# Kernel optimization log

Hardware: AMD Instinct MI355X
Metric: run time of the kernel (lower is better)

## Reference

```python
import jax, jax.numpy as jnp
import numpy as np


def setup_inputs() -> dict:
    key = jax.random.key(0)
    B, C, T = 64, 256, 2048
    X = jax.random.normal(key, (B, C, T), dtype=jnp.float32)
    return {"X": X}


def reference(X) -> jnp.ndarray:
    # torch.cov(correction=0) per sample: rows = variables, cols = observations
    T = X.shape[-1]
    Xc = X - jnp.mean(X, axis=-1, keepdims=True)      # [B, C, T]
    cov = jnp.einsum('bct,bdt->bcd', Xc, Xc) / T       # [B, C, C]
    return cov
```

## Files before the change

kernel.cpp:

```cpp
#include <hip/hip_runtime.h>


#define NB 64
#define NC 256
#define NT 2048
#define NITER 32

typedef __bf16 bf16x8 __attribute__((ext_vector_type(8)));
typedef float  f32x8  __attribute__((ext_vector_type(8)));
typedef float  f32x4  __attribute__((ext_vector_type(4)));

__global__ __launch_bounds__(512, 2) void cov_kernel(const float* __restrict__ X,
                                                     float* __restrict__ out) {
    __shared__ __align__(16) unsigned char smem[68608];
    __bf16* sAB  = (__bf16*)smem;
    float*  redF = (float*)smem;

    const int bid  = blockIdx.x;
    const int xcd  = bid & 7;
    const int g    = bid >> 3;
    const int b    = xcd + 8 * (g >> 2);
    const int q    = g & 3;
    const int row0 = (q >> 1) * 128, col0 = (q & 1) * 128;

    const float* __restrict__ Xb = X + (size_t)b * (NC * NT);

    const int t    = threadIdx.x;
    const int lane = t & 63;
    const int wave = t >> 6;
    const int h    = wave >> 2;
    const int wq   = wave & 3;
    const int wm   = wq >> 1, wn = wq & 1;
    const int quad = lane >> 4;
    const int l16  = lane & 15;

    const int u  = t & 255;
    const int sr = u >> 2;
    const int sc = (u & 3) * 8;
    const float* gA0 = Xb + (size_t)(row0 + sr) * NT + h * (NT / 2) + sc;
    const float* gA1 = gA0 + (size_t)64 * NT;
    const float* gB0 = Xb + (size_t)(col0 + sr) * NT + h * (NT / 2) + sc;
    const float* gB1 = gB0 + (size_t)64 * NT;

    __bf16* sA[2] = { sAB + (0 * 2 + h) * 4096, sAB + (1 * 2 + h) * 4096 };
    __bf16* sB[2] = { sAB + 16384 + (0 * 2 + h) * 4096, sAB + 16384 + (1 * 2 + h) * 4096 };
    const int woff = sr * 32 + sc;

    f32x4 acc[4][4], accRS[4], accCS[4];
#pragma unroll
    for (int i = 0; i < 4; ++i) {
        accRS[i] = (f32x4){0.f, 0.f, 0.f, 0.f};
        accCS[i] = (f32x4){0.f, 0.f, 0.f, 0.f};
#pragma unroll
        for (int j = 0; j < 4; ++j) acc[i][j] = (f32x4){0.f, 0.f, 0.f, 0.f};
    }
    const bf16x8 ones = {(__bf16)1.0f, (__bf16)1.0f, (__bf16)1.0f, (__bf16)1.0f,
                         (__bf16)1.0f, (__bf16)1.0f, (__bf16)1.0f, (__bf16)1.0f};

    f32x8 pA0 = *(const f32x8*)gA0;
    f32x8 pA1 = *(const f32x8*)gA1;
    f32x8 pB0 = *(const f32x8*)gB0;
    f32x8 pB1 = *(const f32x8*)gB1;
    *(bf16x8*)(sA[0] + woff)        = __builtin_convertvector(pA0, bf16x8);
    *(bf16x8*)(sA[0] + woff + 2048) = __builtin_convertvector(pA1, bf16x8);
    *(bf16x8*)(sB[0] + woff)        = __builtin_convertvector(pB0, bf16x8);
    *(bf16x8*)(sB[0] + woff + 2048) = __builtin_convertvector(pB1, bf16x8);
    pA0 = *(const f32x8*)(gA0 + 32);
    pA1 = *(const f32x8*)(gA1 + 32);
    pB0 = *(const f32x8*)(gB0 + 32);
    pB1 = *(const f32x8*)(gB1 + 32);
    __syncthreads();

    const int aBase = (wm * 64 + l16) * 32 + quad * 8;
    const int bBase = (wn * 64 + l16) * 32 + quad * 8;

#pragma unroll 2
    for (int k = 0; k < NITER; ++k) {
        const int cur = k & 1, nxt = cur ^ 1;

        if (k + 1 < NITER) {
            *(bf16x8*)(sA[nxt] + woff)        = __builtin_convertvector(pA0, bf16x8);
            *(bf16x8*)(sA[nxt] + woff + 2048) = __builtin_convertvector(pA1, bf16x8);
            *(bf16x8*)(sB[nxt] + woff)        = __builtin_convertvector(pB0, bf16x8);
            *(bf16x8*)(sB[nxt] + woff + 2048) = __builtin_convertvector(pB1, bf16x8);
        }
        if (k + 2 < NITER) {
            pA0 = *(const f32x8*)(gA0 + (k + 2) * 32);
            pA1 = *(const f32x8*)(gA1 + (k + 2) * 32);
            pB0 = *(const f32x8*)(gB0 + (k + 2) * 32);
            pB1 = *(const f32x8*)(gB1 + (k + 2) * 32);
        }

        bf16x8 aF[4], bF[4];
#pragma unroll
        for (int mt = 0; mt < 4; ++mt)
            aF[mt] = *(const bf16x8*)(sA[cur] + aBase + mt * 16 * 32);
#pragma unroll
        for (int nt = 0; nt < 4; ++nt)
            bF[nt] = *(const bf16x8*)(sB[cur] + bBase + nt * 16 * 32);

#pragma unroll
        for (int mt = 0; mt < 4; ++mt) {
            accRS[mt] = __builtin_amdgcn_mfma_f32_16x16x32_bf16(aF[mt], ones, accRS[mt], 0, 0, 0);
#pragma unroll
            for (int nt = 0; nt < 4; ++nt)
                acc[mt][nt] = __builtin_amdgcn_mfma_f32_16x16x32_bf16(aF[mt], bF[nt], acc[mt][nt], 0, 0, 0);
        }
#pragma unroll
        for (int nt = 0; nt < 4; ++nt)
            accCS[nt] = __builtin_amdgcn_mfma_f32_16x16x32_bf16(ones, bF[nt], accCS[nt], 0, 0, 0);

        __syncthreads();
    }

    float* red = redF + wq * (64 * 65);
    float* rs  = redF + 4 * (64 * 65);
    float* cs  = rs + 256;

    if (h == 1) {
#pragma unroll
        for (int mt = 0; mt < 4; ++mt)
#pragma unroll
            for (int nt = 0; nt < 4; ++nt)
#pragma unroll
                for (int r = 0; r < 4; ++r)
                    red[(mt * 16 + quad * 4 + r) * 65 + nt * 16 + l16] = acc[mt][nt][r];
        if (l16 == 0) {
#pragma unroll
            for (int mt = 0; mt < 4; ++mt)
#pragma unroll
                for (int r = 0; r < 4; ++r)
                    rs[wq * 64 + mt * 16 + quad * 4 + r] = accRS[mt][r];
        }
        if (quad == 0) {
#pragma unroll
            for (int nt = 0; nt < 4; ++nt)
                cs[wq * 64 + nt * 16 + l16] = accCS[nt][0];
        }
    }
    __syncthreads();

    if (h == 0) {
        const float invT = 1.0f / NT;
        float* __restrict__ outB = out + (size_t)b * (NC * NC);
#pragma unroll
        for (int mt = 0; mt < 4; ++mt) {
#pragma unroll
            for (int nt = 0; nt < 4; ++nt) {
#pragma unroll
                for (int r = 0; r < 4; ++r) {
                    const int R = mt * 16 + quad * 4 + r;
                    const int C = nt * 16 + l16;
                    const float tot = red[R * 65 + C] + acc[mt][nt][r];
                    const float Sx  = rs[wq * 64 + R] + accRS[mt][r];
                    const float Sy  = cs[wq * 64 + C] + accCS[nt][0];
                    outB[(size_t)(row0 + wm * 64 + R) * NC + (col0 + wn * 64 + C)] =
                        (tot - Sx * Sy * invT) * invT;
                }
            }
        }
    }
}

extern "C" void kernel_launch(void* const* d_in, const int* in_sizes, int n_in,
                              void* d_out, int out_size, void* d_ws, size_t ws_size,
                              hipStream_t stream) {
    const float* X = (const float*)d_in[0];
    float* out = (float*)d_out;
    (void)in_sizes; (void)n_in; (void)out_size; (void)d_ws; (void)ws_size;
    cov_kernel<<<256, 512, 0, stream>>>(X, out);
}
```

Before: 205.4 us.

## Split-K Gram over full 256x256 tiles with a separate reduction kernel

Each block now computes the full 256x256 Gram matrix for one batch over a quarter of the time axis. Because the tile is symmetric, the row sums equal the column sums, so only column sums are kept. Partial products and sums go to workspace, and a second elementwise kernel adds the slices and applies the mean correction. This cuts global reads of X, which were duplicated across the quadrant tiles before, and drops the LDS reduction, at the cost of writing and re-reading four partial 64x256x256 matrices plus a second launch. If the workspace is too small, the old kernel runs as a fallback.

```diff
diff --git a/kernel.cpp b/kernel.cpp
--- a/kernel.cpp
+++ b/kernel.cpp
@@ -4,101 +4,219 @@
 #define NB 64
 #define NC 256
 #define NT 2048
-#define NITER 32
+#define NSLICE 4
+#define KSL (NT / NSLICE)
+#define NITER (KSL / 32)
+#define PS (NB * NC * NC)
+#define SS (NB * NC)
 
 typedef __bf16 bf16x8 __attribute__((ext_vector_type(8)));
 typedef float  f32x8  __attribute__((ext_vector_type(8)));
 typedef float  f32x4  __attribute__((ext_vector_type(4)));
 
-__global__ __launch_bounds__(512, 2) void cov_kernel(const float* __restrict__ X,
-                                                     float* __restrict__ out) {
+__device__ __forceinline__ void lds_barrier() {
+    asm volatile("s_waitcnt lgkmcnt(0)\n\ts_barrier" ::: "memory");
+}
+
+__global__ __launch_bounds__(512, 2) void cov_gram(const float* __restrict__ X,
+                                                   float* __restrict__ ws) {
+    const int bid   = blockIdx.x;
+    const int b     = bid >> 2;
+    const int slice = bid & 3;
+
+    const float* __restrict__ Xb = X + (size_t)b * (NC * NT) + slice * KSL;
+
+    __shared__ __bf16 sAB[2][NC * 32];
+
+    const int t    = threadIdx.x;
+    const int lane = t & 63;
+    const int wave = t >> 6;
+    const int wm   = wave >> 2;
+    const int wn   = wave & 3;
+    const int quad = lane >> 4;
+    const int l16  = lane & 15;
+
+    const int sr = t >> 2;
+    const int sc = (t & 3) * 8;
+    const float* g0 = Xb + (size_t)sr * NT + sc;
+    const float* g1 = g0 + (size_t)128 * NT;
+    const int woff = sr * 32 + sc;
+
+    f32x4 acc[8][4];
+    f32x4 accCS[4];
+#pragma unroll
+    for (int i = 0; i < 8; ++i)
+#pragma unroll
+        for (int j = 0; j < 4; ++j) acc[i][j] = (f32x4){0.f, 0.f, 0.f, 0.f};
+#pragma unroll
+    for (int j = 0; j < 4; ++j) accCS[j] = (f32x4){0.f, 0.f, 0.f, 0.f};
+
+    const bf16x8 ones = {(__bf16)1.0f, (__bf16)1.0f, (__bf16)1.0f, (__bf16)1.0f,
+                         (__bf16)1.0f, (__bf16)1.0f, (__bf16)1.0f, (__bf16)1.0f};
+
+    f32x8 p0 = *(const f32x8*)g0;
+    f32x8 p1 = *(const f32x8*)g1;
+    *(bf16x8*)(&sAB[0][woff])        = __builtin_convertvector(p0, bf16x8);
+    *(bf16x8*)(&sAB[0][woff + 4096]) = __builtin_convertvector(p1, bf16x8);
+    p0 = *(const f32x8*)(g0 + 32);
+    p1 = *(const f32x8*)(g1 + 32);
+    lds_barrier();
+
+    const int aBase = (wm * 128 + l16) * 32 + quad * 8;
+    const int bBase = (wn * 64 + l16) * 32 + quad * 8;
+
+#pragma unroll 2
+    for (int k = 0; k < NITER; ++k) {
+        const int cur = k & 1, nxt = cur ^ 1;
+
+        if (k + 1 < NITER) {
+            *(bf16x8*)(&sAB[nxt][woff])        = __builtin_convertvector(p0, bf16x8);
+            *(bf16x8*)(&sAB[nxt][woff + 4096]) = __builtin_convertvector(p1, bf16x8);
+        }
+        if (k + 2 < NITER) {
+            p0 = *(const f32x8*)(g0 + (k + 2) * 32);
+            p1 = *(const f32x8*)(g1 + (k + 2) * 32);
+        }
+
+        bf16x8 aF[8], bF[4];
+#pragma unroll
+        for (int mt = 0; mt < 8; ++mt)
+            aF[mt] = *(const bf16x8*)(&sAB[cur][aBase + mt * 16 * 32]);
+#pragma unroll
+        for (int nt = 0; nt < 4; ++nt)
+            bF[nt] = *(const bf16x8*)(&sAB[cur][bBase + nt * 16 * 32]);
+
+#pragma unroll
+        for (int mt = 0; mt < 8; ++mt)
+#pragma unroll
+            for (int nt = 0; nt < 4; ++nt)
+                acc[mt][nt] = __builtin_amdgcn_mfma_f32_16x16x32_bf16(aF[mt], bF[nt], acc[mt][nt], 0, 0, 0);
+        if (wm == 0) {
+#pragma unroll
+            for (int nt = 0; nt < 4; ++nt)
+                accCS[nt] = __builtin_amdgcn_mfma_f32_16x16x32_bf16(ones, bF[nt], accCS[nt], 0, 0, 0);
+        }
+
+        lds_barrier();
+    }
+
+    float* __restrict__ P = ws + (size_t)slice * PS + (size_t)b * (NC * NC);
+#pragma unroll
+    for (int mt = 0; mt < 8; ++mt) {
+        const int rbase = (wm * 128 + mt * 16 + quad * 4) * NC;
+#pragma unroll
+        for (int nt = 0; nt < 4; ++nt) {
+            const int col = wn * 64 + nt * 16 + l16;
+#pragma unroll
+            for (int r = 0; r < 4; ++r)
+                P[rbase + r * NC + col] = acc[mt][nt][r];
+        }
+    }
+    if (wm == 0 && quad == 0) {
+        float* __restrict__ S = ws + (size_t)NSLICE * PS + (size_t)slice * SS + b * NC;
+#pragma unroll
+        for (int nt = 0; nt < 4; ++nt)
+            S[wn * 64 + nt * 16 + l16] = accCS[nt][0];
+    }
+}
+
+__global__ __launch_bounds__(256) void cov_reduce(const float* __restrict__ ws,
+                                                  float* __restrict__ out) {
+    const int tid = blockIdx.x * 256 + threadIdx.x;
+    const int fbase = tid * 16;
+    const int b   = fbase >> 16;
+    const int rem = fbase & 65535;
+    const int r   = rem >> 8;
+    const int c   = rem & 255;
+
+    const float* S = ws + (size_t)NSLICE * PS;
+    float Sx = 0.f;
+    f32x4 Sy[4] = {{0,0,0,0},{0,0,0,0},{0,0,0,0},{0,0,0,0}};
+    f32x4 sP[4] = {{0,0,0,0},{0,0,0,0},{0,0,0,0},{0,0,0,0}};
+#pragma unroll
+    for (int s = 0; s < NSLICE; ++s) {
+        const float* Ps = ws + (size_t)s * PS + fbase;
+        const float* Ss = S + (size_t)s * SS + b * NC;
+        Sx += Ss[r];
+#pragma unroll
+        for (int j = 0; j < 4; ++j) {
+            sP[j] += *(const f32x4*)(Ps + j * 4);
+            Sy[j] += *(const f32x4*)(Ss + c + j * 4);
+        }
+    }
+    const float invT = 1.0f / NT;
+    const float SxT  = Sx * invT;
+#pragma unroll
+    for (int j = 0; j < 4; ++j) {
+        f32x4 v;
+#pragma unroll
+        for (int e = 0; e < 4; ++e) v[e] = (sP[j][e] - SxT * Sy[j][e]) * invT;
+        *(f32x4*)(out + fbase + j * 4) = v;
+    }
+}
+
+__global__ __launch_bounds__(512, 2) void cov_fallback(const float* __restrict__ X,
+                                                       float* __restrict__ out) {
     __shared__ __align__(16) unsigned char smem[68608];
     __bf16* sAB  = (__bf16*)smem;
     float*  redF = (float*)smem;
-
     const int bid  = blockIdx.x;
     const int xcd  = bid & 7;
     const int g    = bid >> 3;
     const int b    = xcd + 8 * (g >> 2);
     const int q    = g & 3;
     const int row0 = (q >> 1) * 128, col0 = (q & 1) * 128;
-
     const float* __restrict__ Xb = X + (size_t)b * (NC * NT);
-
-    const int t    = threadIdx.x;
-    const int lane = t & 63;
-    const int wave = t >> 6;
-    const int h    = wave >> 2;
-    const int wq   = wave & 3;
-    const int wm   = wq >> 1, wn = wq & 1;
-    const int quad = lane >> 4;
-    const int l16  = lane & 15;
-
-    const int u  = t & 255;
-    const int sr = u >> 2;
-    const int sc = (u & 3) * 8;
+    const int t = threadIdx.x, lane = t & 63, wave = t >> 6;
+    const int h = wave >> 2, wq = wave & 3;
+    const int wm = wq >> 1, wn = wq & 1;
+    const int quad = lane >> 4, l16 = lane & 15;
+    const int u = t & 255, sr = u >> 2, sc = (u & 3) * 8;
     const float* gA0 = Xb + (size_t)(row0 + sr) * NT + h * (NT / 2) + sc;
     const float* gA1 = gA0 + (size_t)64 * NT;
     const float* gB0 = Xb + (size_t)(col0 + sr) * NT + h * (NT / 2) + sc;
     const float* gB1 = gB0 + (size_t)64 * NT;
-
     __bf16* sA[2] = { sAB + (0 * 2 + h) * 4096, sAB + (1 * 2 + h) * 4096 };
     __bf16* sB[2] = { sAB + 16384 + (0 * 2 + h) * 4096, sAB + 16384 + (1 * 2 + h) * 4096 };
     const int woff = sr * 32 + sc;
-
     f32x4 acc[4][4], accRS[4], accCS[4];
 #pragma unroll
     for (int i = 0; i < 4; ++i) {
-        accRS[i] = (f32x4){0.f, 0.f, 0.f, 0.f};
-        accCS[i] = (f32x4){0.f, 0.f, 0.f, 0.f};
-#pragma unroll
-        for (int j = 0; j < 4; ++j) acc[i][j] = (f32x4){0.f, 0.f, 0.f, 0.f};
-    }
-    const bf16x8 ones = {(__bf16)1.0f, (__bf16)1.0f, (__bf16)1.0f, (__bf16)1.0f,
-                         (__bf16)1.0f, (__bf16)1.0f, (__bf16)1.0f, (__bf16)1.0f};
-
-    f32x8 pA0 = *(const f32x8*)gA0;
-    f32x8 pA1 = *(const f32x8*)gA1;
-    f32x8 pB0 = *(const f32x8*)gB0;
-    f32x8 pB1 = *(const f32x8*)gB1;
-    *(bf16x8*)(sA[0] + woff)        = __builtin_convertvector(pA0, bf16x8);
-    *(bf16x8*)(sA[0] + woff + 2048) = __builtin_convertvector(pA1, bf16x8);
-    *(bf16x8*)(sB[0] + woff)        = __builtin_convertvector(pB0, bf16x8);
-    *(bf16x8*)(sB[0] + woff + 2048) = __builtin_convertvector(pB1, bf16x8);
-    pA0 = *(const f32x8*)(gA0 + 32);
-    pA1 = *(const f32x8*)(gA1 + 32);
-    pB0 = *(const f32x8*)(gB0 + 32);
-    pB1 = *(const f32x8*)(gB1 + 32);
+        accRS[i] = (f32x4){0.f,0.f,0.f,0.f}; accCS[i] = (f32x4){0.f,0.f,0.f,0.f};
+#pragma unroll
+        for (int j = 0; j < 4; ++j) acc[i][j] = (f32x4){0.f,0.f,0.f,0.f};
+    }
+    const bf16x8 ones = {(__bf16)1.0f,(__bf16)1.0f,(__bf16)1.0f,(__bf16)1.0f,
+                         (__bf16)1.0f,(__bf16)1.0f,(__bf16)1.0f,(__bf16)1.0f};
+    f32x8 pA0 = *(const f32x8*)gA0, pA1 = *(const f32x8*)gA1;
+    f32x8 pB0 = *(const f32x8*)gB0, pB1 = *(const f32x8*)gB1;
+    *(bf16x8*)(sA[0]+woff) = __builtin_convertvector(pA0, bf16x8);
+    *(bf16x8*)(sA[0]+woff+2048) = __builtin_convertvector(pA1, bf16x8);
+    *(bf16x8*)(sB[0]+woff) = __builtin_convertvector(pB0, bf16x8);
+    *(bf16x8*)(sB[0]+woff+2048) = __builtin_convertvector(pB1, bf16x8);
+    pA0 = *(const f32x8*)(gA0+32); pA1 = *(const f32x8*)(gA1+32);
+    pB0 = *(const f32x8*)(gB0+32); pB1 = *(const f32x8*)(gB1+32);
     __syncthreads();
-
     const int aBase = (wm * 64 + l16) * 32 + quad * 8;
     const int bBase = (wn * 64 + l16) * 32 + quad * 8;
-
 #pragma unroll 2
-    for (int k = 0; k < NITER; ++k) {
+    for (int k = 0; k < 32; ++k) {
         const int cur = k & 1, nxt = cur ^ 1;
-
-        if (k + 1 < NITER) {
-            *(bf16x8*)(sA[nxt] + woff)        = __builtin_convertvector(pA0, bf16x8);
-            *(bf16x8*)(sA[nxt] + woff + 2048) = __builtin_convertvector(pA1, bf16x8);
-            *(bf16x8*)(sB[nxt] + woff)        = __builtin_convertvector(pB0, bf16x8);
-            *(bf16x8*)(sB[nxt] + woff + 2048) = __builtin_convertvector(pB1, bf16x8);
-        }
-        if (k + 2 < NITER) {
-            pA0 = *(const f32x8*)(gA0 + (k + 2) * 32);
-            pA1 = *(const f32x8*)(gA1 + (k + 2) * 32);
-            pB0 = *(const f32x8*)(gB0 + (k + 2) * 32);
-            pB1 = *(const f32x8*)(gB1 + (k + 2) * 32);
-        }
-
+        if (k + 1 < 32) {
+            *(bf16x8*)(sA[nxt]+woff) = __builtin_convertvector(pA0, bf16x8);
+            *(bf16x8*)(sA[nxt]+woff+2048) = __builtin_convertvector(pA1, bf16x8);
+            *(bf16x8*)(sB[nxt]+woff) = __builtin_convertvector(pB0, bf16x8);
+            *(bf16x8*)(sB[nxt]+woff+2048) = __builtin_convertvector(pB1, bf16x8);
+        }
+        if (k + 2 < 32) {
+            pA0 = *(const f32x8*)(gA0+(k+2)*32); pA1 = *(const f32x8*)(gA1+(k+2)*32);
+            pB0 = *(const f32x8*)(gB0+(k+2)*32); pB1 = *(const f32x8*)(gB1+(k+2)*32);
+        }
         bf16x8 aF[4], bF[4];
 #pragma unroll
-        for (int mt = 0; mt < 4; ++mt)
-            aF[mt] = *(const bf16x8*)(sA[cur] + aBase + mt * 16 * 32);
-#pragma unroll
-        for (int nt = 0; nt < 4; ++nt)
-            bF[nt] = *(const bf16x8*)(sB[cur] + bBase + nt * 16 * 32);
-
+        for (int mt = 0; mt < 4; ++mt) aF[mt] = *(const bf16x8*)(sA[cur]+aBase+mt*16*32);
+#pragma unroll
+        for (int nt = 0; nt < 4; ++nt) bF[nt] = *(const bf16x8*)(sB[cur]+bBase+nt*16*32);
 #pragma unroll
         for (int mt = 0; mt < 4; ++mt) {
             accRS[mt] = __builtin_amdgcn_mfma_f32_16x16x32_bf16(aF[mt], ones, accRS[mt], 0, 0, 0);
@@ -109,14 +227,11 @@
 #pragma unroll
         for (int nt = 0; nt < 4; ++nt)
             accCS[nt] = __builtin_amdgcn_mfma_f32_16x16x32_bf16(ones, bF[nt], accCS[nt], 0, 0, 0);
-
         __syncthreads();
     }
-
     float* red = redF + wq * (64 * 65);
     float* rs  = redF + 4 * (64 * 65);
     float* cs  = rs + 256;
-
     if (h == 1) {
 #pragma unroll
         for (int mt = 0; mt < 4; ++mt)
@@ -124,41 +239,32 @@
             for (int nt = 0; nt < 4; ++nt)
 #pragma unroll
                 for (int r = 0; r < 4; ++r)
-                    red[(mt * 16 + quad * 4 + r) * 65 + nt * 16 + l16] = acc[mt][nt][r];
-        if (l16 == 0) {
+                    red[(mt*16+quad*4+r)*65 + nt*16+l16] = acc[mt][nt][r];
+        if (l16 == 0)
 #pragma unroll
             for (int mt = 0; mt < 4; ++mt)
 #pragma unroll
-                for (int r = 0; r < 4; ++r)
-                    rs[wq * 64 + mt * 16 + quad * 4 + r] = accRS[mt][r];
-        }
-        if (quad == 0) {
-#pragma unroll
-            for (int nt = 0; nt < 4; ++nt)
-                cs[wq * 64 + nt * 16 + l16] = accCS[nt][0];
-        }
+                for (int r = 0; r < 4; ++r) rs[wq*64+mt*16+quad*4+r] = accRS[mt][r];
+        if (quad == 0)
+#pragma unroll
+            for (int nt = 0; nt < 4; ++nt) cs[wq*64+nt*16+l16] = accCS[nt][0];
     }
     __syncthreads();
-
     if (h == 0) {
         const float invT = 1.0f / NT;
         float* __restrict__ outB = out + (size_t)b * (NC * NC);
 #pragma unroll
-        for (int mt = 0; mt < 4; ++mt) {
-#pragma unroll
-            for (int nt = 0; nt < 4; ++nt) {
+        for (int mt = 0; mt < 4; ++mt)
+#pragma unroll
+            for (int nt = 0; nt < 4; ++nt)
 #pragma unroll
                 for (int r = 0; r < 4; ++r) {
-                    const int R = mt * 16 + quad * 4 + r;
-                    const int C = nt * 16 + l16;
-                    const float tot = red[R * 65 + C] + acc[mt][nt][r];
-                    const float Sx  = rs[wq * 64 + R] + accRS[mt][r];
-                    const float Sy  = cs[wq * 64 + C] + accCS[nt][0];
-                    outB[(size_t)(row0 + wm * 64 + R) * NC + (col0 + wn * 64 + C)] =
-                        (tot - Sx * Sy * invT) * invT;
+                    const int R = mt*16+quad*4+r, C = nt*16+l16;
+                    const float tot = red[R*65+C] + acc[mt][nt][r];
+                    const float Sx = rs[wq*64+R] + accRS[mt][r];
+                    const float Sy = cs[wq*64+C] + accCS[nt][0];
+                    outB[(size_t)(row0+wm*64+R)*NC + (col0+wn*64+C)] = (tot - Sx*Sy*invT)*invT;
                 }
-            }
-        }
     }
 }
 
@@ -167,6 +273,13 @@
                               hipStream_t stream) {
     const float* X = (const float*)d_in[0];
     float* out = (float*)d_out;
-    (void)in_sizes; (void)n_in; (void)out_size; (void)d_ws; (void)ws_size;
-    cov_kernel<<<256, 512, 0, stream>>>(X, out);
-}
+    (void)in_sizes; (void)n_in; (void)out_size;
+    const size_t need = ((size_t)NSLICE * PS + (size_t)NSLICE * SS) * sizeof(float);
+    if (ws_size >= need) {
+        float* ws = (float*)d_ws;
+        cov_gram<<<NB * NSLICE, 512, 0, stream>>>(X, ws);
+        cov_reduce<<<(NB * NC * NC) / (256 * 16), 256, 0, stream>>>(ws, out);
+    } else {
+        cov_fallback<<<256, 512, 0, stream>>>(X, out);
+    }
+}
```

After: 221.0 us. +7.6%, slower.

## Exploit covariance symmetry: compute 3 tiles per batch and mirror off-diagonal

Applied to the files above, without the earlier changes.

Each batch's 256x256 covariance is now covered by three 128x128 tiles (two diagonal, one off-diagonal) rather than four, and the off-diagonal tile is also written transposed into the mirrored position. Diagonal tiles load only one operand and reuse it as both A and B, which cuts global loads and conversions. The LDS row stride is padded to 36 to reduce bank conflicts, and the barriers become explicit lgkmcnt waits. The grid drops from 256 to 192 blocks, so fewer CUs are used, and the transposed store adds an extra sync plus strided writes.

```diff
diff --git a/kernel.cpp b/kernel.cpp
--- a/kernel.cpp
+++ b/kernel.cpp
@@ -5,34 +5,38 @@
 #define NC 256
 #define NT 2048
 #define NITER 32
+#define LSTR 36
+#define HSZ (128 * LSTR)
 
 typedef __bf16 bf16x8 __attribute__((ext_vector_type(8)));
 typedef float  f32x8  __attribute__((ext_vector_type(8)));
 typedef float  f32x4  __attribute__((ext_vector_type(4)));
 
+__device__ __forceinline__ void lds_barrier() {
+    asm volatile("s_waitcnt lgkmcnt(0)\n\ts_barrier" ::: "memory");
+}
+
 __global__ __launch_bounds__(512, 2) void cov_kernel(const float* __restrict__ X,
                                                      float* __restrict__ out) {
-    __shared__ __align__(16) unsigned char smem[68608];
-    __bf16* sAB  = (__bf16*)smem;
-    float*  redF = (float*)smem;
+    __shared__ __align__(16) unsigned char smem[8 * HSZ * 2];
+    __bf16* S = (__bf16*)smem;
 
     const int bid  = blockIdx.x;
     const int xcd  = bid & 7;
-    const int g    = bid >> 3;
-    const int b    = xcd + 8 * (g >> 2);
-    const int q    = g & 3;
-    const int row0 = (q >> 1) * 128, col0 = (q & 1) * 128;
+    const int sidx = bid >> 3;
+    const int b    = xcd + 8 * (sidx / 3);
+    const int type = sidx % 3;
+    const bool offd = (type == 2);
+    const int row0 = (type == 1) ? 128 : 0;
+    const int col0 = (type == 0) ? 0 : 128;
 
     const float* __restrict__ Xb = X + (size_t)b * (NC * NT);
 
-    const int t    = threadIdx.x;
-    const int lane = t & 63;
-    const int wave = t >> 6;
+    const int t = threadIdx.x, lane = t & 63, wave = t >> 6;
     const int h    = wave >> 2;
     const int wq   = wave & 3;
     const int wm   = wq >> 1, wn = wq & 1;
-    const int quad = lane >> 4;
-    const int l16  = lane & 15;
+    const int quad = lane >> 4, l16 = lane & 15;
 
     const int u  = t & 255;
     const int sr = u >> 2;
@@ -42,9 +46,12 @@
     const float* gB0 = Xb + (size_t)(col0 + sr) * NT + h * (NT / 2) + sc;
     const float* gB1 = gB0 + (size_t)64 * NT;
 
-    __bf16* sA[2] = { sAB + (0 * 2 + h) * 4096, sAB + (1 * 2 + h) * 4096 };
-    __bf16* sB[2] = { sAB + 16384 + (0 * 2 + h) * 4096, sAB + 16384 + (1 * 2 + h) * 4096 };
-    const int woff = sr * 32 + sc;
+    const int woff = sr * LSTR + sc;
+    __bf16* wA[2] = { S + (0 + h) * HSZ, S + (2 + h) * HSZ };
+    __bf16* wB[2] = { S + (4 + h) * HSZ, S + (6 + h) * HSZ };
+    const __bf16* rA[2] = { wA[0], wA[1] };
+    const __bf16* rB[2] = { offd ? (const __bf16*)wB[0] : (const __bf16*)wA[0],
+                            offd ? (const __bf16*)wB[1] : (const __bf16*)wA[1] };
 
     f32x4 acc[4][4], accRS[4], accCS[4];
 #pragma unroll
@@ -59,45 +66,50 @@
 
     f32x8 pA0 = *(const f32x8*)gA0;
     f32x8 pA1 = *(const f32x8*)gA1;
-    f32x8 pB0 = *(const f32x8*)gB0;
-    f32x8 pB1 = *(const f32x8*)gB1;
-    *(bf16x8*)(sA[0] + woff)        = __builtin_convertvector(pA0, bf16x8);
-    *(bf16x8*)(sA[0] + woff + 2048) = __builtin_convertvector(pA1, bf16x8);
-    *(bf16x8*)(sB[0] + woff)        = __builtin_convertvector(pB0, bf16x8);
-    *(bf16x8*)(sB[0] + woff + 2048) = __builtin_convertvector(pB1, bf16x8);
+    f32x8 pB0, pB1;
+    if (offd) { pB0 = *(const f32x8*)gB0; pB1 = *(const f32x8*)gB1; }
+    *(bf16x8*)(wA[0] + woff)             = __builtin_convertvector(pA0, bf16x8);
+    *(bf16x8*)(wA[0] + woff + 64 * LSTR) = __builtin_convertvector(pA1, bf16x8);
+    if (offd) {
+        *(bf16x8*)(wB[0] + woff)             = __builtin_convertvector(pB0, bf16x8);
+        *(bf16x8*)(wB[0] + woff + 64 * LSTR) = __builtin_convertvector(pB1, bf16x8);
+    }
     pA0 = *(const f32x8*)(gA0 + 32);
     pA1 = *(const f32x8*)(gA1 + 32);
-    pB0 = *(const f32x8*)(gB0 + 32);
-    pB1 = *(const f32x8*)(gB1 + 32);
-    __syncthreads();
-
-    const int aBase = (wm * 64 + l16) * 32 + quad * 8;
-    const int bBase = (wn * 64 + l16) * 32 + quad * 8;
+    if (offd) { pB0 = *(const f32x8*)(gB0 + 32); pB1 = *(const f32x8*)(gB1 + 32); }
+    lds_barrier();
+
+    const int aBase = (wm * 64 + l16) * LSTR + quad * 8;
+    const int bBase = (wn * 64 + l16) * LSTR + quad * 8;
 
 #pragma unroll 2
     for (int k = 0; k < NITER; ++k) {
         const int cur = k & 1, nxt = cur ^ 1;
 
         if (k + 1 < NITER) {
-            *(bf16x8*)(sA[nxt] + woff)        = __builtin_convertvector(pA0, bf16x8);
-            *(bf16x8*)(sA[nxt] + woff + 2048) = __builtin_convertvector(pA1, bf16x8);
-            *(bf16x8*)(sB[nxt] + woff)        = __builtin_convertvector(pB0, bf16x8);
-            *(bf16x8*)(sB[nxt] + woff + 2048) = __builtin_convertvector(pB1, bf16x8);
+            *(bf16x8*)(wA[nxt] + woff)             = __builtin_convertvector(pA0, bf16x8);
+            *(bf16x8*)(wA[nxt] + woff + 64 * LSTR) = __builtin_convertvector(pA1, bf16x8);
+            if (offd) {
+                *(bf16x8*)(wB[nxt] + woff)             = __builtin_convertvector(pB0, bf16x8);
+                *(bf16x8*)(wB[nxt] + woff + 64 * LSTR) = __builtin_convertvector(pB1, bf16x8);
+            }
         }
         if (k + 2 < NITER) {
             pA0 = *(const f32x8*)(gA0 + (k + 2) * 32);
             pA1 = *(const f32x8*)(gA1 + (k + 2) * 32);
-            pB0 = *(const f32x8*)(gB0 + (k + 2) * 32);
-            pB1 = *(const f32x8*)(gB1 + (k + 2) * 32);
+            if (offd) {
+                pB0 = *(const f32x8*)(gB0 + (k + 2) * 32);
+                pB1 = *(const f32x8*)(gB1 + (k + 2) * 32);
+            }
         }
 
         bf16x8 aF[4], bF[4];
 #pragma unroll
         for (int mt = 0; mt < 4; ++mt)
-            aF[mt] = *(const bf16x8*)(sA[cur] + aBase + mt * 16 * 32);
+            aF[mt] = *(const bf16x8*)(rA[cur] + aBase + mt * 16 * LSTR);
 #pragma unroll
         for (int nt = 0; nt < 4; ++nt)
-            bF[nt] = *(const bf16x8*)(sB[cur] + bBase + nt * 16 * 32);
+            bF[nt] = *(const bf16x8*)(rB[cur] + bBase + nt * 16 * LSTR);
 
 #pragma unroll
         for (int mt = 0; mt < 4; ++mt) {
@@ -110,12 +122,13 @@
         for (int nt = 0; nt < 4; ++nt)
             accCS[nt] = __builtin_amdgcn_mfma_f32_16x16x32_bf16(ones, bF[nt], accCS[nt], 0, 0, 0);
 
-        __syncthreads();
-    }
-
-    float* red = redF + wq * (64 * 65);
-    float* rs  = redF + 4 * (64 * 65);
-    float* cs  = rs + 256;
+        lds_barrier();
+    }
+
+    float* redF = (float*)smem;
+    float* red  = redF + wq * (64 * 65);
+    float* rs   = redF + 4 * (64 * 65);
+    float* cs   = rs + 256;
 
     if (h == 1) {
 #pragma unroll
@@ -125,24 +138,23 @@
 #pragma unroll
                 for (int r = 0; r < 4; ++r)
                     red[(mt * 16 + quad * 4 + r) * 65 + nt * 16 + l16] = acc[mt][nt][r];
-        if (l16 == 0) {
+        if (l16 == 0)
 #pragma unroll
             for (int mt = 0; mt < 4; ++mt)
 #pragma unroll
                 for (int r = 0; r < 4; ++r)
                     rs[wq * 64 + mt * 16 + quad * 4 + r] = accRS[mt][r];
-        }
-        if (quad == 0) {
+        if (quad == 0)
 #pragma unroll
             for (int nt = 0; nt < 4; ++nt)
                 cs[wq * 64 + nt * 16 + l16] = accCS[nt][0];
-        }
     }
     __syncthreads();
 
+    const float invT = 1.0f / NT;
+    float* __restrict__ outB = out + (size_t)b * (NC * NC);
+
     if (h == 0) {
-        const float invT = 1.0f / NT;
-        float* __restrict__ outB = out + (size_t)b * (NC * NC);
 #pragma unroll
         for (int mt = 0; mt < 4; ++mt) {
 #pragma unroll
@@ -154,8 +166,27 @@
                     const float tot = red[R * 65 + C] + acc[mt][nt][r];
                     const float Sx  = rs[wq * 64 + R] + accRS[mt][r];
                     const float Sy  = cs[wq * 64 + C] + accCS[nt][0];
-                    outB[(size_t)(row0 + wm * 64 + R) * NC + (col0 + wn * 64 + C)] =
-                        (tot - Sx * Sy * invT) * invT;
+                    const float val = (tot - Sx * Sy * invT) * invT;
+                    outB[(size_t)(row0 + wm * 64 + R) * NC + (col0 + wn * 64 + C)] = val;
+                    if (offd) red[R * 65 + C] = val;
+                }
+            }
+        }
+    }
+    if (offd) {
+        __syncthreads();
+        if (h == 1) {
+#pragma unroll
+            for (int ci = 0; ci < 4; ++ci) {
+#pragma unroll
+                for (int rj = 0; rj < 4; ++rj) {
+#pragma unroll
+                    for (int e = 0; e < 4; ++e) {
+                        const int C = ci * 16 + quad * 4 + e;
+                        const int R = rj * 16 + l16;
+                        outB[(size_t)(col0 + wn * 64 + C) * NC + (row0 + wm * 64 + R)] =
+                            red[R * 65 + C];
+                    }
                 }
             }
         }
@@ -168,5 +199,5 @@
     const float* X = (const float*)d_in[0];
     float* out = (float*)d_out;
     (void)in_sizes; (void)n_in; (void)out_size; (void)d_ws; (void)ws_size;
-    cov_kernel<<<256, 512, 0, stream>>>(X, out);
+    cov_kernel<<<192, 512, 0, stream>>>(X, out);
 }
```

After: 239.1 us. +16.4%, slower.
